# Performance work log

Measured on AMD Instinct MI355X. Metric: run time of the kernel, lower is better.

Reference implementation:

```python
import jax, jax.numpy as jnp
import numpy as np

NC = 80
REG_MAX = 16          # detect head reg_max; BboxLoss uses REG_MAX-1 = 15
TOPK = 10
ALPHA = 0.5
BETA = 6.0
EPS = 1e-9
HYP_BOX, HYP_CLS, HYP_DFL = 7.5, 0.5, 1.5


def _make_anchors():
    # 640x640 image, strides 8/16/32 -> grids 80/40/20; offset 0.5 (grid units)
    pts, strd = [], []
    for hw, s in ((80, 8.0), (40, 16.0), (20, 32.0)):
        sx = np.arange(hw, dtype=np.float32) + 0.5
        sy, sxg = np.meshgrid(sx, sx, indexing='ij')
        pts.append(np.stack([sxg, sy], -1).reshape(-1, 2))
        strd.append(np.full((hw * hw, 1), s, np.float32))
    return np.concatenate(pts), np.concatenate(strd)


def ciou(box1, box2, eps=1e-7):
    """CIoU, mirrors torch compute_iou (eps added to heights only)."""
    b1x1, b1y1, b1x2, b1y2 = jnp.split(box1, 4, -1)
    b2x1, b2y1, b2x2, b2y2 = jnp.split(box2, 4, -1)
    w1, h1 = b1x2 - b1x1, b1y2 - b1y1 + eps
    w2, h2 = b2x2 - b2x1, b2y2 - b2y1 + eps
    inter = (jnp.clip(jnp.minimum(b1x2, b2x2) - jnp.maximum(b1x1, b2x1), 0)
             * jnp.clip(jnp.minimum(b1y2, b2y2) - jnp.maximum(b1y1, b2y1), 0))
    union = w1 * h1 + w2 * h2 - inter + eps
    iou = inter / union
    cw = jnp.maximum(b1x2, b2x2) - jnp.minimum(b1x1, b2x1)
    ch = jnp.maximum(b1y2, b2y2) - jnp.minimum(b1y1, b2y1)
    c2 = cw ** 2 + ch ** 2 + eps
    rho2 = ((b2x1 + b2x2 - b1x1 - b1x2) ** 2 + (b2y1 + b2y2 - b1y1 - b1y2) ** 2) / 4
    v = (4.0 / np.pi ** 2) * (jnp.arctan(w2 / h2) - jnp.arctan(w1 / h1)) ** 2
    alpha = jax.lax.stop_gradient(v / (v - iou + (1 + eps)))  # torch: with no_grad
    return iou - (rho2 / c2 + v * alpha)


def _assigner(ps, pb, anc, gt_labels, gt_bboxes, mask_gt):
    """TaskAlignedAssigner. ps:[B,A,NC] sigmoid scores, pb:[B,A,4] pixel boxes,
    anc:[A,2] pixel anchor points. Returns (target_bboxes, target_scores, fg_mask)."""
    B, A, _ = ps.shape
    M = gt_bboxes.shape[1]
    lt, rb = gt_bboxes[..., :2], gt_bboxes[..., 2:]                      # [B,M,2]
    deltas = jnp.concatenate([anc[None, None] - lt[:, :, None],
                              rb[:, :, None] - anc[None, None]], -1)     # [B,M,A,4]
    mask_in = deltas.min(-1) > EPS                                       # [B,M,A]
    mgt = mask_in & (mask_gt[:, :, None] > 0)                            # bool [B,M,A]
    mgtf = mgt.astype(ps.dtype)
    # bbox_scores[b,m,a] = ps[b,a,gt_labels[b,m]] where mgt else 0
    bsc = ps[jnp.arange(B)[:, None], :, gt_labels]                       # [B,M,A]
    bbox_scores = jnp.where(mgt, bsc, 0.0)
    ov = jnp.clip(ciou(gt_bboxes[:, :, None], pb[:, None])[..., 0], 0)   # [B,M,A]
    overlaps = jnp.where(mgt, ov, 0.0)
    align = bbox_scores ** ALPHA * overlaps ** BETA
    tkm, tki = jax.lax.top_k(align, TOPK)                                # [B,M,K]
    keep = (tkm > EPS) & jnp.take_along_axis(mgt, tki, -1)
    tki = jnp.where(keep, tki, 0)                                        # masked -> 0 (as torch)
    bidx = jnp.arange(B)[:, None, None]
    midx = jnp.arange(M)[None, :, None]
    cnt = jnp.zeros((B, M, A), jnp.int32).at[bidx, midx, tki].add(1)
    mask_topk = jnp.minimum(cnt, 1).astype(ps.dtype)
    mask_pos = mask_topk * mgtf                                          # [B,M,A]
    fg = mask_pos.sum(-2)                                                # [B,A]
    # resolve anchors assigned to multiple GTs by max overlap (no-op if none)
    multi = fg[:, None, :] > 1
    max_idx = overlaps.argmax(1)                                         # [B,A]
    is_max = (jnp.arange(M)[None, :, None] == max_idx[:, None, :]).astype(mask_pos.dtype)
    mask_pos = jnp.where(multi, is_max, mask_pos)
    fg = mask_pos.sum(-2)
    tgt_idx = mask_pos.argmax(-2)                                        # [B,A]
    tlab = jnp.clip(jnp.take_along_axis(gt_labels, tgt_idx, 1), 0)       # [B,A]
    tbox = jnp.take_along_axis(gt_bboxes, tgt_idx[..., None], 1)         # [B,A,4]
    tscores = jax.nn.one_hot(tlab, NC, dtype=ps.dtype) * (fg[..., None] > 0)
    align = align * mask_pos
    pos_align = align.max(-1, keepdims=True)                             # [B,M,1]
    pos_ov = (overlaps * mask_pos).max(-1, keepdims=True)
    norm = (align * pos_ov / (pos_align + EPS)).max(-2)[..., None]       # [B,A,1]
    return tbox, tscores * norm, fg > 0


def _loss(pred_scores, pred_distri, anchor_points, stride_tensor, gt_bboxes, mask_gt, gt_labels):
    B, A, _ = pred_scores.shape
    # box decode (DFL expectation)
    proj = jnp.arange(REG_MAX, dtype=pred_distri.dtype)
    dist = jax.nn.softmax(pred_distri.reshape(B, A, 4, REG_MAX), -1) @ proj  # [B,A,4]
    lt, rb = dist[..., :2], dist[..., 2:]
    pred_bboxes = jnp.concatenate([anchor_points - lt, anchor_points + rb], -1)  # grid units
    sg = jax.lax.stop_gradient  # assigner is @torch.no_grad
    tbox, tscores, fg = _assigner(sg(jax.nn.sigmoid(pred_scores)),
                                  sg(pred_bboxes * stride_tensor),
                                  anchor_points * stride_tensor,
                                  gt_labels, gt_bboxes, mask_gt)
    tss = jnp.maximum(tscores.sum(), 1.0)
    # BCEWithLogits, sum / tss
    x = pred_scores
    bce = jnp.maximum(x, 0) - x * tscores + jnp.log1p(jnp.exp(-jnp.abs(x)))
    loss_cls = bce.sum() / tss
    # bbox + DFL losses (masked reductions instead of masked_select)
    tbox = tbox / stride_tensor
    weight = tscores.sum(-1)                                             # [B,A]
    fgf = fg.astype(weight.dtype)
    iou = ciou(pred_bboxes, tbox)[..., 0]                                # [B,A]
    loss_iou = ((1.0 - iou) * weight * fgf).sum() / tss
    rm = REG_MAX - 1                                                     # BboxLoss reg_max = 15
    tgt = jnp.clip(jnp.concatenate([anchor_points - tbox[..., :2],
                                    tbox[..., 2:] - anchor_points], -1), 0, rm - 0.01)  # [B,A,4]
    logp = jax.nn.log_softmax(pred_distri.reshape(B, A, 4, REG_MAX), -1)
    tl = tgt.astype(jnp.int32)
    wl = (tl + 1).astype(tgt.dtype) - tgt
    wr = 1.0 - wl
    left = -jnp.take_along_axis(logp, tl[..., None], -1)[..., 0]
    right = -jnp.take_along_axis(logp, (tl + 1)[..., None], -1)[..., 0]
    dfl = (left * wl + right * wr).mean(-1)                              # [B,A]
    loss_dfl = (dfl * weight * fgf).sum() / tss
    return jnp.stack([loss_iou * HYP_BOX, loss_cls * HYP_CLS, loss_dfl * HYP_DFL])


def setup_inputs() -> dict:
    key = jax.random.key(0)
    k0, k1, k2, k3, k4, k5 = jax.random.split(key, 6)
    B, A, M = 32, 8400, 40
    pred_scores = jax.random.normal(k0, (B, A, NC), jnp.float32)
    pred_distri = jax.random.normal(k1, (B, A, 4 * REG_MAX), jnp.float32)
    anc, strd = _make_anchors()
    cxy = jax.random.uniform(k2, (B, M, 2)) * 640.0
    wh = jax.random.uniform(k3, (B, M, 2)) * 150.0 + 10.0
    gt_bboxes = jnp.concatenate([jnp.clip(cxy - wh / 2, 0, 640),
                                 jnp.clip(cxy + wh / 2, 0, 640)], -1)
    mask_gt = (jax.random.uniform(k4, (B, M)) < 0.8).astype(jnp.float32)
    gt_labels = jax.random.randint(k5, (B, M), 0, NC)
    return {"pred_scores": pred_scores, "pred_distri": pred_distri,
            "anchor_points": jnp.asarray(anc), "stride_tensor": jnp.asarray(strd),
            "gt_bboxes": gt_bboxes, "mask_gt": mask_gt, "gt_labels": gt_labels}


def reference(pred_scores, pred_distri, anchor_points, stride_tensor, gt_bboxes, mask_gt, gt_labels):
    return _loss(pred_scores, pred_distri, anchor_points, stride_tensor, gt_bboxes, mask_gt, gt_labels)
```

## Files before the change

kernel.cpp:

```cpp
#include <hip/hip_runtime.h>
#include <math.h>

#define B_    32
#define A_    8400
#define M_    40
#define NC_   80
#define TOPK_ 10
#define EPS_  1e-9f

#define NTHR  524288

__device__ __forceinline__ float ciou_f(float b1x1, float b1y1, float b1x2, float b1y2,
                                        float b2x1, float b2y1, float b2x2, float b2y2) {
    const float eps = 1e-7f;
    float w1 = b1x2 - b1x1, h1 = b1y2 - b1y1 + eps;
    float w2 = b2x2 - b2x1, h2 = b2y2 - b2y1 + eps;
    float iw = fminf(b1x2, b2x2) - fmaxf(b1x1, b2x1);
    float ih = fminf(b1y2, b2y2) - fmaxf(b1y1, b2y1);
    float inter = fmaxf(iw, 0.f) * fmaxf(ih, 0.f);
    float uni = w1 * h1 + w2 * h2 - inter + eps;
    float iou = inter / uni;
    float cw = fmaxf(b1x2, b2x2) - fminf(b1x1, b2x1);
    float ch = fmaxf(b1y2, b2y2) - fminf(b1y1, b2y1);
    float c2 = cw * cw + ch * ch + eps;
    float dx = b2x1 + b2x2 - b1x1 - b1x2;
    float dy = b2y1 + b2y2 - b1y1 - b1y2;
    float rho2 = (dx * dx + dy * dy) * 0.25f;
    float da = atanf(w2 / h2) - atanf(w1 / h1);
    float v = 0.4052847345693511f * da * da;
    float alpha = v / (v - iou + 1.f + eps);
    return iou - (rho2 / c2 + v * alpha);
}

__device__ __forceinline__ void anchor_of(int a, float& ax, float& ay, float& s) {
    if (a < 6400)      { s = 8.f;  int r = a;        ax = (float)(r % 80) + 0.5f; ay = (float)(r / 80) + 0.5f; }
    else if (a < 8000) { s = 16.f; int r = a - 6400; ax = (float)(r % 40) + 0.5f; ay = (float)(r / 40) + 0.5f; }
    else               { s = 32.f; int r = a - 8000; ax = (float)(r % 20) + 0.5f; ay = (float)(r / 20) + 0.5f; }
}

__device__ __forceinline__ float ov_at2(const float* __restrict__ pb,
                                        float g0, float g1, float g2, float g3,
                                        int b, int a) {
    float ax, ay, s; anchor_of(a, ax, ay, s);
    float axp = ax * s, ayp = ay * s;
    if (!((axp - g0) > EPS_ && (ayp - g1) > EPS_ && (g2 - axp) > EPS_ && (g3 - ayp) > EPS_))
        return 0.f;
    const float4 p = *(const float4*)(pb + ((size_t)b * A_ + a) * 4);
    float c = ciou_f(g0, g1, g2, g3, p.x * s, p.y * s, p.z * s, p.w * s);
    return fmaxf(c, 0.f);
}

__device__ __forceinline__ unsigned long long shflxor_u64(unsigned long long v, int m) {
    int lo = __shfl_xor((int)(unsigned)(v & 0xffffffffull), m, 64);
    int hi = __shfl_xor((int)(unsigned)(v >> 32), m, 64);
    return ((unsigned long long)(unsigned)hi << 32) | (unsigned)lo;
}

__device__ __forceinline__ float qsum_dpp(float v) {
    int y = __builtin_amdgcn_update_dpp(0, __float_as_int(v), 0xB1, 0xF, 0xF, true);
    float r = v + __int_as_float(y);
    int z = __builtin_amdgcn_update_dpp(0, __float_as_int(r), 0x4E, 0xF, 0xF, true);
    return r + __int_as_float(z);
}

template <int CTRL>
__device__ __forceinline__ unsigned long long dpp64(unsigned long long v) {
    unsigned lo = (unsigned)__builtin_amdgcn_update_dpp(0, (int)(unsigned)v, CTRL, 0xF, 0xF, true);
    unsigned hi = (unsigned)__builtin_amdgcn_update_dpp(0, (int)(unsigned)(v >> 32), CTRL, 0xF, 0xF, true);
    return ((unsigned long long)hi << 32) | lo;
}

__device__ __forceinline__ unsigned long long max64(unsigned long long a, unsigned long long b) {
    return a > b ? a : b;
}

__device__ __forceinline__ unsigned long long swz16_64(unsigned long long v) {
    unsigned lo = (unsigned)__builtin_amdgcn_ds_swizzle((int)(unsigned)v, 0x401F);
    unsigned hi = (unsigned)__builtin_amdgcn_ds_swizzle((int)(unsigned)(v >> 32), 0x401F);
    return ((unsigned long long)hi << 32) | lo;
}

__device__ __forceinline__ unsigned long long wave_max_u64(unsigned long long w) {
    w = max64(w, dpp64<0xB1>(w));
    w = max64(w, dpp64<0x4E>(w));
    w = max64(w, dpp64<0x141>(w));
    w = max64(w, dpp64<0x140>(w));
    w = max64(w, swz16_64(w));
    w = max64(w, shflxor_u64(w, 32));
    return w;
}

__device__ __forceinline__ void dfl_quad(float4 v, int f, float* __restrict__ pb) {
    int q = f & 3;
    float e0 = __expf(v.x), e1 = __expf(v.y), e2 = __expf(v.z), e3 = __expf(v.w);
    float se = e0 + e1 + e2 + e3;
    float sd = e1 + 2.f * e2 + 3.f * e3 + (float)(4 * q) * se;
    se = qsum_dpp(se);
    sd = qsum_dpp(sd);
    float dist = sd / se;
    int di = __float_as_int(dist);
    float d1 = __int_as_float(__builtin_amdgcn_update_dpp(0, di, 0x104, 0xF, 0xF, true));
    float d2 = __int_as_float(__builtin_amdgcn_update_dpp(0, di, 0x108, 0xF, 0xF, true));
    float d3 = __int_as_float(__builtin_amdgcn_update_dpp(0, di, 0x10C, 0xF, 0xF, true));
    if ((f & 15) == 0) {
        int aidx = f >> 4;
        int a = aidx % A_;
        float ax, ay, s; anchor_of(a, ax, ay, s);
        ((float4*)pb)[aidx] = make_float4(ax - dist, ay - d1, ax + d2, ay + d3);
    }
}

__device__ __forceinline__ float bce4(float4 x) {
    return fmaxf(x.x, 0.f) + __logf(1.f + __expf(-fabsf(x.x)))
         + fmaxf(x.y, 0.f) + __logf(1.f + __expf(-fabsf(x.y)))
         + fmaxf(x.z, 0.f) + __logf(1.f + __expf(-fabsf(x.z)))
         + fmaxf(x.w, 0.f) + __logf(1.f + __expf(-fabsf(x.w)));
}

__global__ void k_stream(const float4* __restrict__ d4,
                         const float4* __restrict__ s4,
                         float* __restrict__ pb,
                         unsigned long long* __restrict__ abits64,
                         unsigned long long* __restrict__ ovmax,
                         float* __restrict__ acc) {
    const int tid0 = blockIdx.x * blockDim.x + threadIdx.x;
    if (tid0 < B_ * A_) {
        abits64[tid0] = 0ull;
        ovmax[tid0] = 0x00000000FFFFFFFFull;
    }
    {
        const int NF4 = B_ * A_ * 16;
        float4 v0 = d4[tid0];
        float4 v1 = d4[tid0 + NTHR];
        float4 v2 = d4[tid0 + 2 * NTHR];
        float4 v3 = d4[tid0 + 3 * NTHR];
        float4 v4 = d4[tid0 + 4 * NTHR];
        float4 v5 = d4[tid0 + 5 * NTHR];
        float4 v6 = d4[tid0 + 6 * NTHR];
        float4 v7 = d4[tid0 + 7 * NTHR];
        dfl_quad(v0, tid0, pb);
        dfl_quad(v1, tid0 + NTHR, pb);
        dfl_quad(v2, tid0 + 2 * NTHR, pb);
        dfl_quad(v3, tid0 + 3 * NTHR, pb);
        dfl_quad(v4, tid0 + 4 * NTHR, pb);
        dfl_quad(v5, tid0 + 5 * NTHR, pb);
        dfl_quad(v6, tid0 + 6 * NTHR, pb);
        dfl_quad(v7, tid0 + 7 * NTHR, pb);
        int f8 = tid0 + 8 * NTHR;
        if (f8 < NF4) dfl_quad(d4[f8], f8, pb);
    }
    float sum = 0.f;
    {
        const int N4 = B_ * A_ * (NC_ / 4);
        float4 x0 = s4[tid0];
        float4 x1 = s4[tid0 + NTHR];
        float4 x2 = s4[tid0 + 2 * NTHR];
        float4 x3 = s4[tid0 + 3 * NTHR];
        float4 x4 = s4[tid0 + 4 * NTHR];
        float4 x5 = s4[tid0 + 5 * NTHR];
        float4 x6 = s4[tid0 + 6 * NTHR];
        float4 x7 = s4[tid0 + 7 * NTHR];
        sum += bce4(x0); sum += bce4(x1); sum += bce4(x2); sum += bce4(x3);
        sum += bce4(x4); sum += bce4(x5); sum += bce4(x6); sum += bce4(x7);
        float4 x8 = s4[tid0 + 8 * NTHR];
        float4 x9 = s4[tid0 + 9 * NTHR];
        sum += bce4(x8); sum += bce4(x9);
        int f10 = tid0 + 10 * NTHR;
        if (f10 < N4) sum += bce4(s4[f10]);
    }
    __shared__ float sh[256];
    sh[threadIdx.x] = sum; __syncthreads();
    for (int s = 128; s > 0; s >>= 1) {
        if (threadIdx.x < s) sh[threadIdx.x] += sh[threadIdx.x + s];
        __syncthreads();
    }
    if (threadIdx.x == 0) atomicAdd(&acc[1], sh[0]);
}

__global__ __launch_bounds__(64) void k_aligntopk(
    const float* __restrict__ scores, const float* __restrict__ pb,
    const float* __restrict__ gt, const float* __restrict__ mgt,
    const int* __restrict__ glab, unsigned int* __restrict__ abits,
    unsigned long long* __restrict__ ovmax) {
    int bm = blockIdx.x;
    if (mgt[bm] <= 0.f) return;
    int b = bm / M_, m = bm % M_;
    int lab = glab[bm];
    const float g0 = gt[bm * 4 + 0], g1 = gt[bm * 4 + 1];
    const float g2 = gt[bm * 4 + 2], g3 = gt[bm * 4 + 3];
    int lane = threadIdx.x;

    const int   Wl[3]  = { 80, 40, 20 };
    const int   Bs[3]  = { 0, 6400, 8000 };
    const float Sl[3]  = { 8.f, 16.f, 32.f };
    int jlo[3], ilo[3], rw[3], cnt[3];
#pragma unroll
    for (int l = 0; l < 3; l++) {
        float s = Sl[l]; int W = Wl[l];
        int jl = max(0, (int)floorf(g0 / s - 0.5f) - 1);
        int jh = min(W - 1, (int)ceilf(g2 / s - 0.5f) + 1);
        int il = max(0, (int)floorf(g1 / s - 0.5f) - 1);
        int ih = min(W - 1, (int)ceilf(g3 / s - 0.5f) + 1);
        int w = jh - jl + 1, h = ih - il + 1;
        jlo[l] = jl; ilo[l] = il; rw[l] = max(w, 0);
        cnt[l] = (w > 0 && h > 0) ? w * h : 0;
    }
    int c01 = cnt[0] + cnt[1];
    int tot = c01 + cnt[2];

    unsigned long long t[TOPK_];
#pragma unroll
    for (int k = 0; k < TOPK_; k++) t[k] = 0ull;

    for (int c = lane; c < tot; c += 64) {
        int l = (c < cnt[0]) ? 0 : ((c < c01) ? 1 : 2);
        int r = c - ((l == 0) ? 0 : ((l == 1) ? cnt[0] : c01));
        int w = rw[l];
        int di = r / w, dj = r - di * w;
        int i = ilo[l] + di, j = jlo[l] + dj;
        float s = Sl[l];
        float ax = ((float)j + 0.5f) * s;
        float ay = ((float)i + 0.5f) * s;
        if (!((ax - g0) > EPS_ && (ay - g1) > EPS_ && (g2 - ax) > EPS_ && (g3 - ay) > EPS_))
            continue;
        int a = Bs[l] + i * Wl[l] + j;
        const float4 p = *(const float4*)(pb + ((size_t)b * A_ + a) * 4);
        float sc = scores[((size_t)b * A_ + a) * NC_ + lab];
        float ci = ciou_f(g0, g1, g2, g3, p.x * s, p.y * s, p.z * s, p.w * s);
        float ov = fmaxf(ci, 0.f);
        float al = 0.f;
        if (ov > 0.f) {
            unsigned long long opk = ((unsigned long long)__float_as_uint(ov) << 32)
                                     | (unsigned)(~(unsigned)m);
            atomicMax(&ovmax[(size_t)b * A_ + a], opk);
            float bs = 1.f / (1.f + __expf(-sc));
            float o2 = ov * ov;
            al = sqrtf(bs) * o2 * o2 * o2;
        }
        unsigned long long pkd = ((unsigned long long)__float_as_uint(al) << 32)
                                 | (unsigned)(~(unsigned)a);
        if (pkd > t[TOPK_ - 1]) {
            unsigned long long cv = pkd;
#pragma unroll
            for (int k = 0; k < TOPK_; k++) {
                bool g = cv > t[k];
                unsigned long long o = t[k];
                t[k] = g ? cv : o;
                cv   = g ? o : cv;
            }
        }
    }

    unsigned long long mysel = 0ull;
#pragma unroll
    for (int k = 0; k < TOPK_; k++) {
        unsigned long long w = wave_max_u64(t[0]);
        if (lane == k) mysel = w;
        if (w != 0ull && t[0] == w) {
#pragma unroll
            for (int q = 0; q < TOPK_ - 1; q++) t[q] = t[q + 1];
            t[TOPK_ - 1] = 0ull;
        }
    }

    float sval = __uint_as_float((unsigned)(mysel >> 32));
    int   sidx = (int)(~(unsigned)mysel);
    unsigned int bit = 1u << (m & 31);
    int word = (m >= 32) ? 1 : 0;
    bool keep = (lane < TOPK_) && (sval > EPS_);
    if (keep) atomicOr(&abits[2 * ((size_t)b * A_ + sidx) + word], bit);
    unsigned long long kb = __ballot(keep);
    if (lane == 0 && __popcll(kb) < TOPK_) {
        float ax = 4.f, ay = 4.f;
        if ((ax - g0) > EPS_ && (ay - g1) > EPS_ && (g2 - ax) > EPS_ && (g3 - ay) > EPS_)
            atomicOr(&abits[2 * ((size_t)b * A_) + word], bit);
    }
}

__global__ __launch_bounds__(256) void k_R(
    const unsigned int* __restrict__ abits,
    const unsigned long long* __restrict__ ovmax,
    const float* __restrict__ pb,
    const float* __restrict__ scores, const float* __restrict__ gt,
    const int* __restrict__ glab,
    int* __restrict__ tgti, float* __restrict__ alv,
    int* __restrict__ pa_g, int* __restrict__ po_g) {
    int idx = blockIdx.x * blockDim.x + threadIdx.x;
    if (idx >= B_ * A_) return;
    unsigned int lo = abits[2 * idx], hi = abits[2 * idx + 1];
    int fg = __popc(lo) + __popc(hi);
    if (fg == 0) { tgti[idx] = -1; return; }
    int b = idx / A_, a = idx % A_;
    int tgt; float ov;
    if (fg > 1) {
        unsigned long long pk = ovmax[idx];
        tgt = (int)(~(unsigned)(pk & 0xffffffffull));
        ov  = __uint_as_float((unsigned)(pk >> 32));
    } else {
        tgt = lo ? (__ffs(lo) - 1) : (32 + __ffs(hi) - 1);
        int bmi = b * M_ + tgt;
        ov = ov_at2(pb, gt[bmi * 4], gt[bmi * 4 + 1], gt[bmi * 4 + 2], gt[bmi * 4 + 3], b, a);
    }
    float al = 0.f;
    if (ov > 0.f) {
        int lab = glab[b * M_ + tgt];
        float sc = scores[(size_t)idx * NC_ + lab];
        float bs = 1.f / (1.f + __expf(-sc));
        float o2 = ov * ov;
        al = sqrtf(bs) * o2 * o2 * o2;
    }
    tgti[idx] = tgt;
    alv[idx] = al;
    int bmi = b * M_ + tgt;
    atomicMax(&pa_g[bmi], __float_as_int(al));
    atomicMax(&po_g[bmi], __float_as_int(ov));
}

__global__ __launch_bounds__(256) void k_S(
    const int* __restrict__ tgti, const float* __restrict__ alv,
    const int* __restrict__ pa_g, const int* __restrict__ po_g,
    const float* __restrict__ scores, const float* __restrict__ pb,
    const float* __restrict__ gt, const int* __restrict__ glab,
    const float* __restrict__ distri, float* __restrict__ acc) {
    int idx = blockIdx.x * blockDim.x + threadIdx.x;
    float ts = 0.f, cs = 0.f, liou = 0.f, ldfl = 0.f;
    if (idx < B_ * A_) {
        int tgt = tgti[idx];
        if (tgt >= 0) {
            int b = idx / A_, a = idx % A_;
            int bmi = b * M_ + tgt;
            float al = alv[idx];
            float pa = __int_as_float(pa_g[bmi]);
            float po = __int_as_float(po_g[bmi]);
            float nv = al * po / (pa + EPS_);
            ts = nv;
            int lab = max(glab[bmi], 0);
            float sc = scores[(size_t)idx * NC_ + lab];
            cs = -sc * nv;
            float ax, ay, s; anchor_of(a, ax, ay, s);
            const float* g = gt + (size_t)bmi * 4;
            float t0 = g[0] / s, t1 = g[1] / s, t2 = g[2] / s, t3 = g[3] / s;
            const float4 p = *(const float4*)(pb + (size_t)idx * 4);
            float iou = ciou_f(p.x, p.y, p.z, p.w, t0, t1, t2, t3);
            liou = (1.f - iou) * nv;
            float tg[4] = { ax - t0, ay - t1, t2 - ax, t3 - ay };
            const float* dd = distri + (size_t)idx * 64;
            float dfl = 0.f;
#pragma unroll
            for (int sd = 0; sd < 4; sd++) {
                float tvv = fminf(fmaxf(tg[sd], 0.f), 14.99f);
                int tl = (int)tvv;
                float wl = (float)(tl + 1) - tvv;
                float wr = 1.f - wl;
                const float* xx = dd + sd * 16;
                float mx = xx[0];
#pragma unroll
                for (int j = 1; j < 16; j++) mx = fmaxf(mx, xx[j]);
                float se = 0.f;
#pragma unroll
                for (int j = 0; j < 16; j++) se += __expf(xx[j] - mx);
                float lse = mx + __logf(se);
                dfl += (lse - xx[tl]) * wl + (lse - xx[tl + 1]) * wr;
            }
            ldfl = dfl * 0.25f * nv;
        }
    }
    __shared__ float r0[256], r1[256], r2[256], r3[256];
    int tid = threadIdx.x;
    r0[tid] = ts; r1[tid] = cs; r2[tid] = liou; r3[tid] = ldfl;
    __syncthreads();
    for (int s = 128; s > 0; s >>= 1) {
        if (tid < s) {
            r0[tid] += r0[tid + s]; r1[tid] += r1[tid + s];
            r2[tid] += r2[tid + s]; r3[tid] += r3[tid + s];
        }
        __syncthreads();
    }
    if (tid == 0) {
        atomicAdd(&acc[0], r0[0]); atomicAdd(&acc[1], r1[0]);
        atomicAdd(&acc[2], r2[0]); atomicAdd(&acc[3], r3[0]);
    }
}

__global__ void k_final(const float* __restrict__ acc, float* __restrict__ out) {
    if (threadIdx.x == 0) {
        float tss = fmaxf(acc[0], 1.f);
        out[0] = acc[2] / tss * 7.5f;
        out[1] = acc[1] / tss * 0.5f;
        out[2] = acc[3] / tss * 1.5f;
    }
}

extern "C" void kernel_launch(void* const* d_in, const int* in_sizes, int n_in,
                              void* d_out, int out_size, void* d_ws, size_t ws_size,
                              hipStream_t stream) {
    const float* scores = (const float*)d_in[0];
    const float* distri = (const float*)d_in[1];
    const float* gtb    = (const float*)d_in[4];
    const float* mgt    = (const float*)d_in[5];
    const int*   glab   = (const int*)d_in[6];
    float* out = (float*)d_out;

    unsigned long long* ovmax = (unsigned long long*)d_ws;
    float* pb    = (float*)(ovmax + (size_t)B_ * A_);
    float* alv   = pb + (size_t)B_ * A_ * 4;
    int*   tgti  = (int*)(alv + (size_t)B_ * A_);
    float* acc   = (float*)(tgti + (size_t)B_ * A_);
    int*   pa_g  = (int*)(acc + 4);
    int*   po_g  = pa_g + B_ * M_;
    unsigned int* abits = (unsigned int*)(po_g + B_ * M_);

    size_t zero_bytes = (4 + 2 * B_ * M_) * sizeof(int);
    hipMemsetAsync(acc, 0, zero_bytes, stream);

    k_stream<<<2048, 256, 0, stream>>>((const float4*)distri, (const float4*)scores, pb,
                                       (unsigned long long*)abits, ovmax, acc);
    k_aligntopk<<<B_ * M_, 64, 0, stream>>>(scores, pb, gtb, mgt, glab, abits, ovmax);
    k_R<<<1050, 256, 0, stream>>>(abits, ovmax, pb, scores, gtb, glab, tgti, alv, pa_g, po_g);
    k_S<<<1050, 256, 0, stream>>>(tgti, alv, pa_g, po_g, scores, pb, gtb, glab, distri, acc);
    k_final<<<1, 64, 0, stream>>>(acc, out);
    (void)in_sizes; (void)n_in; (void)out_size; (void)ws_size;
}
```

Baseline: 284.0 us.

## Move BCE sum into final loss kernel and widen top-k blocks to four waves

The full-tensor BCE reduction over the scores moves out of the first streaming kernel and into k_S, where each thread sums the BCE of its own anchor's 80-class row. This is meant to shorten the first kernel and reuse the score-row access k_S already makes. The per-GT top-k kernel now runs four waves per block instead of one, and the per-wave top-10 candidates are merged through shared memory by wave 0. The risk is that k_S now does 80-wide strided row reads per thread, which coalesce less well than the old flat float4 stream.

```diff
diff --git a/kernel.cpp b/kernel.cpp
--- a/kernel.cpp
+++ b/kernel.cpp
@@ -117,78 +117,51 @@
          + fmaxf(x.w, 0.f) + __logf(1.f + __expf(-fabsf(x.w)));
 }
 
-__global__ void k_stream(const float4* __restrict__ d4,
-                         const float4* __restrict__ s4,
-                         float* __restrict__ pb,
-                         unsigned long long* __restrict__ abits64,
-                         unsigned long long* __restrict__ ovmax,
-                         float* __restrict__ acc) {
+__global__ void k_init_dfl(const float4* __restrict__ d4,
+                           float* __restrict__ pb,
+                           unsigned long long* __restrict__ abits64,
+                           unsigned long long* __restrict__ ovmax) {
     const int tid0 = blockIdx.x * blockDim.x + threadIdx.x;
     if (tid0 < B_ * A_) {
         abits64[tid0] = 0ull;
         ovmax[tid0] = 0x00000000FFFFFFFFull;
     }
-    {
-        const int NF4 = B_ * A_ * 16;
-        float4 v0 = d4[tid0];
-        float4 v1 = d4[tid0 + NTHR];
-        float4 v2 = d4[tid0 + 2 * NTHR];
-        float4 v3 = d4[tid0 + 3 * NTHR];
-        float4 v4 = d4[tid0 + 4 * NTHR];
-        float4 v5 = d4[tid0 + 5 * NTHR];
-        float4 v6 = d4[tid0 + 6 * NTHR];
-        float4 v7 = d4[tid0 + 7 * NTHR];
-        dfl_quad(v0, tid0, pb);
-        dfl_quad(v1, tid0 + NTHR, pb);
-        dfl_quad(v2, tid0 + 2 * NTHR, pb);
-        dfl_quad(v3, tid0 + 3 * NTHR, pb);
-        dfl_quad(v4, tid0 + 4 * NTHR, pb);
-        dfl_quad(v5, tid0 + 5 * NTHR, pb);
-        dfl_quad(v6, tid0 + 6 * NTHR, pb);
-        dfl_quad(v7, tid0 + 7 * NTHR, pb);
-        int f8 = tid0 + 8 * NTHR;
-        if (f8 < NF4) dfl_quad(d4[f8], f8, pb);
-    }
-    float sum = 0.f;
-    {
-        const int N4 = B_ * A_ * (NC_ / 4);
-        float4 x0 = s4[tid0];
-        float4 x1 = s4[tid0 + NTHR];
-        float4 x2 = s4[tid0 + 2 * NTHR];
-        float4 x3 = s4[tid0 + 3 * NTHR];
-        float4 x4 = s4[tid0 + 4 * NTHR];
-        float4 x5 = s4[tid0 + 5 * NTHR];
-        float4 x6 = s4[tid0 + 6 * NTHR];
-        float4 x7 = s4[tid0 + 7 * NTHR];
-        sum += bce4(x0); sum += bce4(x1); sum += bce4(x2); sum += bce4(x3);
-        sum += bce4(x4); sum += bce4(x5); sum += bce4(x6); sum += bce4(x7);
-        float4 x8 = s4[tid0 + 8 * NTHR];
-        float4 x9 = s4[tid0 + 9 * NTHR];
-        sum += bce4(x8); sum += bce4(x9);
-        int f10 = tid0 + 10 * NTHR;
-        if (f10 < N4) sum += bce4(s4[f10]);
-    }
-    __shared__ float sh[256];
-    sh[threadIdx.x] = sum; __syncthreads();
-    for (int s = 128; s > 0; s >>= 1) {
-        if (threadIdx.x < s) sh[threadIdx.x] += sh[threadIdx.x + s];
-        __syncthreads();
-    }
-    if (threadIdx.x == 0) atomicAdd(&acc[1], sh[0]);
-}
-
-__global__ __launch_bounds__(64) void k_aligntopk(
+    const int NF4 = B_ * A_ * 16;
+    float4 v0 = d4[tid0];
+    float4 v1 = d4[tid0 + NTHR];
+    float4 v2 = d4[tid0 + 2 * NTHR];
+    float4 v3 = d4[tid0 + 3 * NTHR];
+    float4 v4 = d4[tid0 + 4 * NTHR];
+    float4 v5 = d4[tid0 + 5 * NTHR];
+    float4 v6 = d4[tid0 + 6 * NTHR];
+    float4 v7 = d4[tid0 + 7 * NTHR];
+    dfl_quad(v0, tid0, pb);
+    dfl_quad(v1, tid0 + NTHR, pb);
+    dfl_quad(v2, tid0 + 2 * NTHR, pb);
+    dfl_quad(v3, tid0 + 3 * NTHR, pb);
+    dfl_quad(v4, tid0 + 4 * NTHR, pb);
+    dfl_quad(v5, tid0 + 5 * NTHR, pb);
+    dfl_quad(v6, tid0 + 6 * NTHR, pb);
+    dfl_quad(v7, tid0 + 7 * NTHR, pb);
+    int f8 = tid0 + 8 * NTHR;
+    if (f8 < NF4) dfl_quad(d4[f8], f8, pb);
+}
+
+__global__ __launch_bounds__(256) void k_aligntopk(
     const float* __restrict__ scores, const float* __restrict__ pb,
     const float* __restrict__ gt, const float* __restrict__ mgt,
     const int* __restrict__ glab, unsigned int* __restrict__ abits,
     unsigned long long* __restrict__ ovmax) {
+    __shared__ unsigned long long sh[4 * TOPK_];
     int bm = blockIdx.x;
     if (mgt[bm] <= 0.f) return;
     int b = bm / M_, m = bm % M_;
     int lab = glab[bm];
     const float g0 = gt[bm * 4 + 0], g1 = gt[bm * 4 + 1];
     const float g2 = gt[bm * 4 + 2], g3 = gt[bm * 4 + 3];
-    int lane = threadIdx.x;
+    int tid  = threadIdx.x;
+    int lane = tid & 63;
+    int wv   = tid >> 6;
 
     const int   Wl[3]  = { 80, 40, 20 };
     const int   Bs[3]  = { 0, 6400, 8000 };
@@ -212,7 +185,7 @@
 #pragma unroll
     for (int k = 0; k < TOPK_; k++) t[k] = 0ull;
 
-    for (int c = lane; c < tot; c += 64) {
+    for (int c = tid; c < tot; c += 256) {
         int l = (c < cnt[0]) ? 0 : ((c < c01) ? 1 : 2);
         int r = c - ((l == 0) ? 0 : ((l == 1) ? cnt[0] : c01));
         int w = rw[l];
@@ -262,9 +235,21 @@
             t[TOPK_ - 1] = 0ull;
         }
     }
-
-    float sval = __uint_as_float((unsigned)(mysel >> 32));
-    int   sidx = (int)(~(unsigned)mysel);
+    if (lane < TOPK_) sh[wv * TOPK_ + lane] = mysel;
+    __syncthreads();
+    if (wv != 0) return;
+
+    unsigned long long val = (lane < 4 * TOPK_) ? sh[lane] : 0ull;
+    unsigned long long fin = 0ull;
+#pragma unroll
+    for (int k = 0; k < TOPK_; k++) {
+        unsigned long long w = wave_max_u64(val);
+        if (lane == k) fin = w;
+        if (w != 0ull && val == w) val = 0ull;
+    }
+
+    float sval = __uint_as_float((unsigned)(fin >> 32));
+    int   sidx = (int)(~(unsigned)fin);
     unsigned int bit = 1u << (m & 31);
     int word = (m >= 32) ? 1 : 0;
     bool keep = (lane < TOPK_) && (sval > EPS_);
@@ -325,6 +310,11 @@
     int idx = blockIdx.x * blockDim.x + threadIdx.x;
     float ts = 0.f, cs = 0.f, liou = 0.f, ldfl = 0.f;
     if (idx < B_ * A_) {
+        const float4* srow = (const float4*)(scores + (size_t)idx * NC_);
+        float bsum = 0.f;
+#pragma unroll
+        for (int c4 = 0; c4 < NC_ / 4; ++c4) bsum += bce4(srow[c4]);
+        cs = bsum;
         int tgt = tgti[idx];
         if (tgt >= 0) {
             int b = idx / A_, a = idx % A_;
@@ -336,7 +326,7 @@
             ts = nv;
             int lab = max(glab[bmi], 0);
             float sc = scores[(size_t)idx * NC_ + lab];
-            cs = -sc * nv;
+            cs -= sc * nv;
             float ax, ay, s; anchor_of(a, ax, ay, s);
             const float* g = gt + (size_t)bmi * 4;
             float t0 = g[0] / s, t1 = g[1] / s, t2 = g[2] / s, t3 = g[3] / s;
@@ -413,9 +403,9 @@
     size_t zero_bytes = (4 + 2 * B_ * M_) * sizeof(int);
     hipMemsetAsync(acc, 0, zero_bytes, stream);
 
-    k_stream<<<2048, 256, 0, stream>>>((const float4*)distri, (const float4*)scores, pb,
-                                       (unsigned long long*)abits, ovmax, acc);
-    k_aligntopk<<<B_ * M_, 64, 0, stream>>>(scores, pb, gtb, mgt, glab, abits, ovmax);
+    k_init_dfl<<<2048, 256, 0, stream>>>((const float4*)distri, pb,
+                                         (unsigned long long*)abits, ovmax);
+    k_aligntopk<<<B_ * M_, 256, 0, stream>>>(scores, pb, gtb, mgt, glab, abits, ovmax);
     k_R<<<1050, 256, 0, stream>>>(abits, ovmax, pb, scores, gtb, glab, tgti, alv, pa_g, po_g);
     k_S<<<1050, 256, 0, stream>>>(tgti, alv, pa_g, po_g, scores, pb, gtb, glab, distri, acc);
     k_final<<<1, 64, 0, stream>>>(acc, out);
```

Result: no change. 280.5 us (-1.2%).

## Fold per-GT normalization into final reduction and widen topk block to four waves

Applied to the files above, without the earlier changes.

The normalization factor po/pa is constant for each ground truth, so per-anchor loss terms can be summed per GT weighted by the raw alignment and scaled only at the end. This lets the R and S kernels merge into one pass, removing the tgti/alv round-trip and a kernel launch. k_final now does the per-GT scaling and reduction. The topk kernel also moves from one wave to four waves per GT, merging the partial top-k lists through shared memory. The cost is many float atomicAdds on per-GT sums, which can contend and changes the summation order.

```diff
diff --git a/kernel.cpp b/kernel.cpp
--- a/kernel.cpp
+++ b/kernel.cpp
@@ -177,18 +177,21 @@
     if (threadIdx.x == 0) atomicAdd(&acc[1], sh[0]);
 }
 
-__global__ __launch_bounds__(64) void k_aligntopk(
+__global__ __launch_bounds__(256) void k_aligntopk(
     const float* __restrict__ scores, const float* __restrict__ pb,
     const float* __restrict__ gt, const float* __restrict__ mgt,
     const int* __restrict__ glab, unsigned int* __restrict__ abits,
     unsigned long long* __restrict__ ovmax) {
+    __shared__ unsigned long long sh[4 * TOPK_];
     int bm = blockIdx.x;
     if (mgt[bm] <= 0.f) return;
     int b = bm / M_, m = bm % M_;
     int lab = glab[bm];
     const float g0 = gt[bm * 4 + 0], g1 = gt[bm * 4 + 1];
     const float g2 = gt[bm * 4 + 2], g3 = gt[bm * 4 + 3];
-    int lane = threadIdx.x;
+    int tid  = threadIdx.x;
+    int lane = tid & 63;
+    int wv   = tid >> 6;
 
     const int   Wl[3]  = { 80, 40, 20 };
     const int   Bs[3]  = { 0, 6400, 8000 };
@@ -212,7 +215,7 @@
 #pragma unroll
     for (int k = 0; k < TOPK_; k++) t[k] = 0ull;
 
-    for (int c = lane; c < tot; c += 64) {
+    for (int c = tid; c < tot; c += 256) {
         int l = (c < cnt[0]) ? 0 : ((c < c01) ? 1 : 2);
         int r = c - ((l == 0) ? 0 : ((l == 1) ? cnt[0] : c01));
         int w = rw[l];
@@ -262,9 +265,21 @@
             t[TOPK_ - 1] = 0ull;
         }
     }
-
-    float sval = __uint_as_float((unsigned)(mysel >> 32));
-    int   sidx = (int)(~(unsigned)mysel);
+    if (lane < TOPK_) sh[wv * TOPK_ + lane] = mysel;
+    __syncthreads();
+    if (wv != 0) return;
+
+    unsigned long long val = (lane < 4 * TOPK_) ? sh[lane] : 0ull;
+    unsigned long long fin = 0ull;
+#pragma unroll
+    for (int k = 0; k < TOPK_; k++) {
+        unsigned long long w = wave_max_u64(val);
+        if (lane == k) fin = w;
+        if (w != 0ull && val == w) val = 0ull;
+    }
+
+    float sval = __uint_as_float((unsigned)(fin >> 32));
+    int   sidx = (int)(~(unsigned)fin);
     unsigned int bit = 1u << (m & 31);
     int word = (m >= 32) ? 1 : 0;
     bool keep = (lane < TOPK_) && (sval > EPS_);
@@ -282,14 +297,14 @@
     const unsigned long long* __restrict__ ovmax,
     const float* __restrict__ pb,
     const float* __restrict__ scores, const float* __restrict__ gt,
-    const int* __restrict__ glab,
-    int* __restrict__ tgti, float* __restrict__ alv,
-    int* __restrict__ pa_g, int* __restrict__ po_g) {
+    const int* __restrict__ glab, const float* __restrict__ distri,
+    int* __restrict__ pa_g, int* __restrict__ po_g,
+    float* __restrict__ gsum) {
     int idx = blockIdx.x * blockDim.x + threadIdx.x;
     if (idx >= B_ * A_) return;
     unsigned int lo = abits[2 * idx], hi = abits[2 * idx + 1];
     int fg = __popc(lo) + __popc(hi);
-    if (fg == 0) { tgti[idx] = -1; return; }
+    if (fg == 0) return;
     int b = idx / A_, a = idx % A_;
     int tgt; float ov;
     if (fg > 1) {
@@ -298,76 +313,71 @@
         ov  = __uint_as_float((unsigned)(pk >> 32));
     } else {
         tgt = lo ? (__ffs(lo) - 1) : (32 + __ffs(hi) - 1);
-        int bmi = b * M_ + tgt;
-        ov = ov_at2(pb, gt[bmi * 4], gt[bmi * 4 + 1], gt[bmi * 4 + 2], gt[bmi * 4 + 3], b, a);
-    }
+        int bmi0 = b * M_ + tgt;
+        ov = ov_at2(pb, gt[bmi0 * 4], gt[bmi0 * 4 + 1], gt[bmi0 * 4 + 2], gt[bmi0 * 4 + 3], b, a);
+    }
+    int bmi = b * M_ + tgt;
     float al = 0.f;
     if (ov > 0.f) {
-        int lab = glab[b * M_ + tgt];
+        int lab = glab[bmi];
         float sc = scores[(size_t)idx * NC_ + lab];
         float bs = 1.f / (1.f + __expf(-sc));
         float o2 = ov * ov;
         al = sqrtf(bs) * o2 * o2 * o2;
     }
-    tgti[idx] = tgt;
-    alv[idx] = al;
-    int bmi = b * M_ + tgt;
     atomicMax(&pa_g[bmi], __float_as_int(al));
     atomicMax(&po_g[bmi], __float_as_int(ov));
-}
-
-__global__ __launch_bounds__(256) void k_S(
-    const int* __restrict__ tgti, const float* __restrict__ alv,
-    const int* __restrict__ pa_g, const int* __restrict__ po_g,
-    const float* __restrict__ scores, const float* __restrict__ pb,
-    const float* __restrict__ gt, const int* __restrict__ glab,
-    const float* __restrict__ distri, float* __restrict__ acc) {
-    int idx = blockIdx.x * blockDim.x + threadIdx.x;
-    float ts = 0.f, cs = 0.f, liou = 0.f, ldfl = 0.f;
-    if (idx < B_ * A_) {
-        int tgt = tgti[idx];
-        if (tgt >= 0) {
-            int b = idx / A_, a = idx % A_;
-            int bmi = b * M_ + tgt;
-            float al = alv[idx];
-            float pa = __int_as_float(pa_g[bmi]);
-            float po = __int_as_float(po_g[bmi]);
-            float nv = al * po / (pa + EPS_);
-            ts = nv;
-            int lab = max(glab[bmi], 0);
-            float sc = scores[(size_t)idx * NC_ + lab];
-            cs = -sc * nv;
-            float ax, ay, s; anchor_of(a, ax, ay, s);
-            const float* g = gt + (size_t)bmi * 4;
-            float t0 = g[0] / s, t1 = g[1] / s, t2 = g[2] / s, t3 = g[3] / s;
-            const float4 p = *(const float4*)(pb + (size_t)idx * 4);
-            float iou = ciou_f(p.x, p.y, p.z, p.w, t0, t1, t2, t3);
-            liou = (1.f - iou) * nv;
-            float tg[4] = { ax - t0, ay - t1, t2 - ax, t3 - ay };
-            const float* dd = distri + (size_t)idx * 64;
-            float dfl = 0.f;
-#pragma unroll
-            for (int sd = 0; sd < 4; sd++) {
-                float tvv = fminf(fmaxf(tg[sd], 0.f), 14.99f);
-                int tl = (int)tvv;
-                float wl = (float)(tl + 1) - tvv;
-                float wr = 1.f - wl;
-                const float* xx = dd + sd * 16;
-                float mx = xx[0];
-#pragma unroll
-                for (int j = 1; j < 16; j++) mx = fmaxf(mx, xx[j]);
-                float se = 0.f;
-#pragma unroll
-                for (int j = 0; j < 16; j++) se += __expf(xx[j] - mx);
-                float lse = mx + __logf(se);
-                dfl += (lse - xx[tl]) * wl + (lse - xx[tl + 1]) * wr;
-            }
-            ldfl = dfl * 0.25f * nv;
+    if (al > 0.f) {
+        int lab2 = max(glab[bmi], 0);
+        float sc2 = scores[(size_t)idx * NC_ + lab2];
+        float ax, ay, s; anchor_of(a, ax, ay, s);
+        const float* g = gt + (size_t)bmi * 4;
+        float t0 = g[0] / s, t1 = g[1] / s, t2 = g[2] / s, t3 = g[3] / s;
+        const float4 p = *(const float4*)(pb + (size_t)idx * 4);
+        float iou = ciou_f(p.x, p.y, p.z, p.w, t0, t1, t2, t3);
+        float tg4[4] = { ax - t0, ay - t1, t2 - ax, t3 - ay };
+        const float* dd = distri + (size_t)idx * 64;
+        float dfl = 0.f;
+#pragma unroll
+        for (int sd = 0; sd < 4; sd++) {
+            float tvv = fminf(fmaxf(tg4[sd], 0.f), 14.99f);
+            int tl = (int)tvv;
+            float wl = (float)(tl + 1) - tvv;
+            float wr = 1.f - wl;
+            const float* xx = dd + sd * 16;
+            float mx = xx[0];
+#pragma unroll
+            for (int j = 1; j < 16; j++) mx = fmaxf(mx, xx[j]);
+            float se = 0.f;
+#pragma unroll
+            for (int j = 0; j < 16; j++) se += __expf(xx[j] - mx);
+            float lse = mx + __logf(se);
+            dfl += (lse - xx[tl]) * wl + (lse - xx[tl + 1]) * wr;
         }
+        atomicAdd(&gsum[bmi * 4 + 0], al);
+        atomicAdd(&gsum[bmi * 4 + 1], al * sc2);
+        atomicAdd(&gsum[bmi * 4 + 2], al * (1.f - iou));
+        atomicAdd(&gsum[bmi * 4 + 3], al * dfl * 0.25f);
+    }
+}
+
+__global__ __launch_bounds__(256) void k_final(
+    const float* __restrict__ acc, const int* __restrict__ pa_g,
+    const int* __restrict__ po_g, const float* __restrict__ gsum,
+    float* __restrict__ out) {
+    int tid = threadIdx.x;
+    float ts = 0.f, cls = 0.f, li = 0.f, ld = 0.f;
+    for (int g = tid; g < B_ * M_; g += 256) {
+        float pa = __int_as_float(pa_g[g]);
+        float po = __int_as_float(po_g[g]);
+        float f = po / (pa + EPS_);
+        ts  += f * gsum[g * 4 + 0];
+        cls += f * gsum[g * 4 + 1];
+        li  += f * gsum[g * 4 + 2];
+        ld  += f * gsum[g * 4 + 3];
     }
     __shared__ float r0[256], r1[256], r2[256], r3[256];
-    int tid = threadIdx.x;
-    r0[tid] = ts; r1[tid] = cs; r2[tid] = liou; r3[tid] = ldfl;
+    r0[tid] = ts; r1[tid] = cls; r2[tid] = li; r3[tid] = ld;
     __syncthreads();
     for (int s = 128; s > 0; s >>= 1) {
         if (tid < s) {
@@ -377,17 +387,10 @@
         __syncthreads();
     }
     if (tid == 0) {
-        atomicAdd(&acc[0], r0[0]); atomicAdd(&acc[1], r1[0]);
-        atomicAdd(&acc[2], r2[0]); atomicAdd(&acc[3], r3[0]);
-    }
-}
-
-__global__ void k_final(const float* __restrict__ acc, float* __restrict__ out) {
-    if (threadIdx.x == 0) {
-        float tss = fmaxf(acc[0], 1.f);
-        out[0] = acc[2] / tss * 7.5f;
-        out[1] = acc[1] / tss * 0.5f;
-        out[2] = acc[3] / tss * 1.5f;
+        float tss = fmaxf(r0[0], 1.f);
+        out[0] = r2[0] / tss * 7.5f;
+        out[1] = (acc[1] - r1[0]) / tss * 0.5f;
+        out[2] = r3[0] / tss * 1.5f;
     }
 }
 
@@ -403,21 +406,20 @@
 
     unsigned long long* ovmax = (unsigned long long*)d_ws;
     float* pb    = (float*)(ovmax + (size_t)B_ * A_);
-    float* alv   = pb + (size_t)B_ * A_ * 4;
-    int*   tgti  = (int*)(alv + (size_t)B_ * A_);
-    float* acc   = (float*)(tgti + (size_t)B_ * A_);
+    float* acc   = pb + (size_t)B_ * A_ * 4;
     int*   pa_g  = (int*)(acc + 4);
     int*   po_g  = pa_g + B_ * M_;
-    unsigned int* abits = (unsigned int*)(po_g + B_ * M_);
-
-    size_t zero_bytes = (4 + 2 * B_ * M_) * sizeof(int);
+    float* gsum  = (float*)(po_g + B_ * M_);
+    unsigned int* abits = (unsigned int*)(gsum + (size_t)B_ * M_ * 4);
+
+    size_t zero_bytes = (4 + 2 * B_ * M_ + 4 * B_ * M_) * sizeof(float);
     hipMemsetAsync(acc, 0, zero_bytes, stream);
 
     k_stream<<<2048, 256, 0, stream>>>((const float4*)distri, (const float4*)scores, pb,
                                        (unsigned long long*)abits, ovmax, acc);
-    k_aligntopk<<<B_ * M_, 64, 0, stream>>>(scores, pb, gtb, mgt, glab, abits, ovmax);
-    k_R<<<1050, 256, 0, stream>>>(abits, ovmax, pb, scores, gtb, glab, tgti, alv, pa_g, po_g);
-    k_S<<<1050, 256, 0, stream>>>(tgti, alv, pa_g, po_g, scores, pb, gtb, glab, distri, acc);
-    k_final<<<1, 64, 0, stream>>>(acc, out);
+    k_aligntopk<<<B_ * M_, 256, 0, stream>>>(scores, pb, gtb, mgt, glab, abits, ovmax);
+    k_R<<<1050, 256, 0, stream>>>(abits, ovmax, pb, scores, gtb, glab, distri,
+                                  pa_g, po_g, gsum);
+    k_final<<<1, 256, 0, stream>>>(acc, pa_g, po_g, gsum, out);
     (void)in_sizes; (void)n_in; (void)out_size; (void)ws_size;
 }
```

Result: faster. 230.0 us (-19.0%).
